# Kernel optimization log

Hardware: AMD Instinct MI355X
Metric: run time of the kernel (lower is better)

## Reference

```python
import jax, jax.numpy as jnp
import numpy as np
from jax import lax

# ---- config (mirrors init_kwargs) ----
B, CIN, T, WIDTH = 32, 8, 256, 128
COUT = 64
K = (5, 5)
PAD = (2, 2)            # ceil((k-1)*dilation/2) per dim
OUT_W = 128             # output_shape
EPS = 1e-8
BETA0 = 0.9             # beta 'constant' init, one_per_layer
B0 = 1.0                # b 'constant' init
SIGMA0 = 10.0
MAX_SPK = 3.0           # Max_spikes_per_run


@jax.custom_vjp
def spike_fn(mthr, sigma):
    # Surrogate Heaviside: hard threshold fwd, sigmoid-derivative surrogate bwd.
    return (mthr > 0).astype(mthr.dtype)

def _spike_fwd(mthr, sigma):
    return spike_fn(mthr, sigma), (mthr, sigma)

def _spike_bwd(res, g):
    mthr, sigma = res
    sg = jax.nn.sigmoid(sigma * mthr)
    return (g * sigma * sg * (1.0 - sg), jnp.zeros_like(sigma))

spike_fn.defvjp(_spike_fwd, _spike_bwd)


def setup_inputs() -> dict:
    key = jax.random.key(0)
    kx, kw = jax.random.split(key)
    x = jax.random.normal(kx, (B, CIN, T, WIDTH), dtype=jnp.float32)
    w_std = 1.0 * np.sqrt(1.0 / (CIN * K[0] * K[1]))
    w = jax.random.normal(kw, (COUT, CIN, K[0], K[1]), dtype=jnp.float32) * w_std
    b = jnp.full((COUT,), B0, dtype=jnp.float32)          # clamped >= 0
    beta = jnp.array([BETA0], dtype=jnp.float32)           # one_per_layer, clamped to [0,1]
    sigma = jnp.array([SIGMA0], dtype=jnp.float32)         # surrogate_sigma_mode 'one'
    return {"x": x, "w": w, "b": b, "beta": beta, "sigma": sigma}


def _forward(x, w, b, beta, sigma):
    # conv over (time, width) with 'same'-style padding, then truncate width
    conv_x = lax.conv_general_dilated(
        x, w, window_strides=(1, 1),
        padding=((PAD[0], PAD[0]), (PAD[1], PAD[1])),
        rhs_dilation=(1, 1),
        dimension_numbers=("NCHW", "OIHW", "NCHW"))
    conv_x = conv_x[:, :, :, :OUT_W]                      # [B, COUT, T, OUT_W]

    d = jnp.einsum("oikl,eikl->oe", w, w)                 # lateral matrix [COUT, COUT]
    norm = jnp.sum(w * w, axis=(1, 2, 3))                 # [COUT]
    inv_norm = 1.0 / (norm + EPS)
    beta_s = beta[0]

    conv_seq = jnp.transpose(conv_x, (2, 0, 1, 3))        # [T, B, COUT, OUT_W]

    def step(carry, inp_t):
        mem, spk, prev = carry
        rst = jnp.einsum("bcw,cd->bdw", spk, d)           # lateral reset
        # Leaky neuron, soft reset
        mem = (mem - rst) * beta_s + inp_t * (1.0 - beta_s)
        mthr = mem * inv_norm[None, :, None] - b[None, :, None]
        s = (MAX_SPK - prev) * spike_fn(mthr, sigma)      # spike_limit=True
        prev = prev + s
        return (mem, s, prev), s

    zeros = jnp.zeros((B, COUT, OUT_W), dtype=x.dtype)
    (_, _, _), spk_rec = lax.scan(step, (zeros, zeros, zeros), conv_seq)
    # spk_rec: [T, B, COUT, OUT_W]

    loss = 0.5 * jnp.mean(spk_rec ** 2)                   # 'squared'
    spk_spread = jnp.max(jnp.sum(spk_rec, axis=(1, 2, 3))) / (B * COUT * OUT_W)  # 'max'

    output = jnp.transpose(spk_rec, (1, 2, 0, 3))         # [B, COUT, T, OUT_W]
    return output, loss, spk_spread


def reference(x, w, b, beta, sigma):
    return _forward(x, w, b, beta, sigma)
```

## Files before the change

kernel.cpp:

```cpp
#include <hip/hip_runtime.h>
#include <cstdint>
#include <math.h>


#define NB 32
#define NC 8
#define NT 256
#define NW 128
#define NO 64
#define WT 16
#define TC 8
#define NROWS 12
#define NCHUNK (NT / TC)
#define XCOLS 20
#define XTILE (NC * NROWS * XCOLS)

__global__ __launch_bounds__(1024)
void prep_kernel(const float* __restrict__ w, float* __restrict__ d3,
                 float* __restrict__ invn, unsigned int* __restrict__ gfires)
{
    __shared__ float wsh[NO * 200];
    const int tid = threadIdx.x;
    for (int i = tid; i < NO * 200; i += 1024) wsh[i] = w[i];
    if (tid < NT) gfires[tid] = 0u;
    __syncthreads();
#pragma unroll
    for (int p = 0; p < 4; ++p) {
        int idx = p * 1024 + tid;
        int o = idx >> 6, e = idx & 63;
        float acc = 0.0f;
        for (int i = 0; i < 200; i += 4) {
            float4 av = *(const float4*)&wsh[o * 200 + i];
            float4 bv = *(const float4*)&wsh[e * 200 + i];
            acc += av.x * bv.x + av.y * bv.y + av.z * bv.z + av.w * bv.w;
        }
        d3[idx] = 3.0f * acc;
        if (o == e) invn[o] = 1.0f / (acc + 1e-8f);
    }
}

__global__ __launch_bounds__(512, 1)
void spk_kernel(const float* __restrict__ x, const float* __restrict__ wglob,
                const float* __restrict__ bias, const float* __restrict__ beta_p,
                const float* __restrict__ d3g, const float* __restrict__ invng,
                float* __restrict__ out, unsigned int* __restrict__ gfires)
{
    __shared__ float wsm[NC * 25 * NO];
    __shared__ float d3s[NO * NO];
    __shared__ float xsh[2][NC][NROWS][XCOLS];
    __shared__ unsigned short tf[2][NO][8];
    __shared__ unsigned int sf[NT];

    const int tid  = threadIdx.x;
    const int lane = tid & 63;
    const int wv   = tid >> 6;
    const int bb   = blockIdx.x >> 3;
    const int w0   = (blockIdx.x & 7) * WT;

    for (int i = tid; i < NC * 25 * NO; i += 512) {
        int co = i & 63; int r = i >> 6;
        int kw = r % 5; int r2 = r / 5; int kt = r2 % 5; int c = r2 / 5;
        wsm[i] = wglob[((co * NC + c) * 5 + kt) * 5 + kw];
    }
    for (int i = tid; i < NO * NO; i += 512) d3s[i] = d3g[i];
    for (int i = tid; i < NT; i += 512) sf[i] = 0u;

    const size_t xbbase = (size_t)bb * NC * NT * NW;

    const float* pf_ptr[4];
    int  pf_idx[4];
    int  pf_row[4];
    bool pf_okw[4];
#pragma unroll
    for (int k = 0; k < 4; ++k) {
        int i = tid + k * 512;
        if (i < XTILE) {
            int c = i / (NROWS * XCOLS); int rem = i - c * (NROWS * XCOLS);
            int row = rem / XCOLS; int col = rem - row * XCOLS;
            int wg = w0 + col - 2;
            pf_idx[k] = i; pf_row[k] = row;
            pf_okw[k] = (wg >= 0 && wg < NW);
            pf_ptr[k] = x + xbbase + ((size_t)c * NT + 6 + row) * NW + (wg < 0 ? 0 : wg);
        } else { pf_idx[k] = -1; pf_row[k] = 0; pf_okw[k] = false; pf_ptr[k] = x; }
    }

    const int sq = tid & 3;
    const int srow = tid >> 2;
    int    sp_tfidx[4];
    int    sp_tt[4];
    float* sp_out[4];
#pragma unroll
    for (int p = 0; p < 4; ++p) {
        int rowi = p * 128 + srow;
        int co = rowi >> 3, tt = rowi & 7;
        sp_tfidx[p] = co * 8 + sq * 2;
        sp_tt[p] = tt;
        sp_out[p] = out + (((size_t)(bb * NO + co) * NT + tt) * NW + w0 + sq * 4);
    }

#pragma unroll
    for (int k = 0; k < 4; ++k) {
        int i = tid + k * 512;
        if (i < XTILE) {
            int c = i / (NROWS * XCOLS); int rem = i - c * (NROWS * XCOLS);
            int row = rem / XCOLS; int col = rem - row * XCOLS;
            int tg = row - 2, wg = w0 + col - 2;
            float v = 0.0f;
            if (tg >= 0 && tg < NT && wg >= 0 && wg < NW)
                v = x[xbbase + ((size_t)c * NT + tg) * NW + wg];
            (&xsh[0][0][0][0])[i] = v;
        }
    }

    const float invn = invng[lane];
    const float bco  = bias[lane];
    const float beta = beta_p[0];
    const float omb  = 1.0f - beta;

    float mem0 = 0.f, mem1 = 0.f;
    unsigned int fired = 0u;
    unsigned long long pm0 = 0ull, pm1 = 0ull;

    __syncthreads();

#pragma unroll 1
    for (int ch = 0; ch < NCHUNK; ++ch) {
        const int buf = ch & 1;
        const int tbase = ch * TC;

        float sr[4];
        if (ch + 1 < NCHUNK) {
#pragma unroll
            for (int k = 0; k < 4; ++k) {
                float v = 0.0f;
                int tg = (ch << 3) + 6 + pf_row[k];
                if (pf_okw[k] && tg < NT)
                    v = pf_ptr[k][(size_t)ch * (TC * NW)];
                sr[k] = v;
            }
        }

        if (ch > 0) {
            const unsigned short* tfp = &tf[buf ^ 1][0][0];
            const size_t oadv = (size_t)(ch - 1) * (TC * NW);
#pragma unroll
            for (int p = 0; p < 4; ++p) {
                unsigned int codes = *(const unsigned int*)(tfp + sp_tfidx[p]);
                unsigned int tt = (unsigned)sp_tt[p];
                float4 v;
                v.x = (((codes      ) & 0xffu) == tt) ? 3.0f : 0.0f;
                v.y = (((codes >>  8) & 0xffu) == tt) ? 3.0f : 0.0f;
                v.z = (((codes >> 16) & 0xffu) == tt) ? 3.0f : 0.0f;
                v.w = (((codes >> 24) & 0xffu) == tt) ? 3.0f : 0.0f;
                *(float4*)(sp_out[p] + oadv) = v;
            }
        }

        float acc[TC][2];
#pragma unroll
        for (int t = 0; t < TC; ++t) { acc[t][0] = 0.f; acc[t][1] = 0.f; }

#pragma unroll 2
        for (int c = 0; c < NC; ++c) {
            float2 xr[NROWS][3];
#pragma unroll
            for (int r = 0; r < NROWS; ++r) {
                const float* base = &xsh[buf][c][r][2 * wv];
                xr[r][0] = *(const float2*)(base);
                xr[r][1] = *(const float2*)(base + 2);
                xr[r][2] = *(const float2*)(base + 4);
            }
#pragma unroll
            for (int kt = 0; kt < 5; ++kt) {
                const float* wp = &wsm[((c * 5 + kt) * 5) * 64 + lane];
                float wk0 = wp[0], wk1 = wp[64], wk2 = wp[128], wk3 = wp[192], wk4 = wp[256];
#pragma unroll
                for (int t = 0; t < TC; ++t) {
                    float2 a = xr[t + kt][0], b2 = xr[t + kt][1], c2 = xr[t + kt][2];
                    float u0 = acc[t][0], u1 = acc[t][1];
                    u0 = fmaf(wk0, a.x,  u0);
                    u0 = fmaf(wk1, a.y,  u0);
                    u0 = fmaf(wk2, b2.x, u0);
                    u0 = fmaf(wk3, b2.y, u0);
                    u0 = fmaf(wk4, c2.x, u0);
                    u1 = fmaf(wk0, a.y,  u1);
                    u1 = fmaf(wk1, b2.x, u1);
                    u1 = fmaf(wk2, b2.y, u1);
                    u1 = fmaf(wk3, c2.x, u1);
                    u1 = fmaf(wk4, c2.y, u1);
                    acc[t][0] = u0; acc[t][1] = u1;
                }
            }
        }

        unsigned int tfc0 = 0xffu, tfc1 = 0xffu;
#pragma unroll
        for (int tt = 0; tt < TC; ++tt) {
            float r0 = 0.f, r1 = 0.f;
            if (pm0 | pm1) {
                unsigned long long m = pm0;
                while (m) { int c = __builtin_ctzll(m); m &= m - 1; r0 += d3s[c * 64 + lane]; }
                m = pm1;
                while (m) { int c = __builtin_ctzll(m); m &= m - 1; r1 += d3s[c * 64 + lane]; }
            }
            mem0 = (mem0 - r0) * beta + acc[tt][0] * omb;
            mem1 = (mem1 - r1) * beta + acc[tt][1] * omb;
            bool f0 = !(fired & 1u) && (mem0 * invn - bco > 0.0f);
            bool f1 = !(fired & 2u) && (mem1 * invn - bco > 0.0f);
            pm0 = __ballot(f0);
            pm1 = __ballot(f1);
            if (f0) { fired |= 1u; tfc0 = (unsigned)tt; }
            if (f1) { fired |= 2u; tfc1 = (unsigned)tt; }
            unsigned int cnt = (unsigned)(__popcll(pm0) + __popcll(pm1));
            if (lane == 0 && cnt) atomicAdd(&sf[tbase + tt], cnt);
        }
        tf[buf][lane][wv] = (unsigned short)(tfc0 | (tfc1 << 8));

        if (ch + 1 < NCHUNK) {
            float* dst = &xsh[buf ^ 1][0][0][0];
#pragma unroll
            for (int k = 0; k < 4; ++k) {
                if (pf_idx[k] >= 0) dst[pf_idx[k]] = sr[k];
            }
        }
        __syncthreads();
    }

    {
        const unsigned short* tfp = &tf[(NCHUNK - 1) & 1][0][0];
        const size_t oadv = (size_t)(NCHUNK - 1) * (TC * NW);
#pragma unroll
        for (int p = 0; p < 4; ++p) {
            unsigned int codes = *(const unsigned int*)(tfp + sp_tfidx[p]);
            unsigned int tt = (unsigned)sp_tt[p];
            float4 v;
            v.x = (((codes      ) & 0xffu) == tt) ? 3.0f : 0.0f;
            v.y = (((codes >>  8) & 0xffu) == tt) ? 3.0f : 0.0f;
            v.z = (((codes >> 16) & 0xffu) == tt) ? 3.0f : 0.0f;
            v.w = (((codes >> 24) & 0xffu) == tt) ? 3.0f : 0.0f;
            *(float4*)(sp_out[p] + oadv) = v;
        }
    }

    if (tid < NT) atomicAdd(&gfires[tid], sf[tid]);
}

__global__ __launch_bounds__(256)
void fin_kernel(const unsigned int* __restrict__ gfires, float* __restrict__ out)
{
    const int tid = threadIdx.x;
    unsigned int v = gfires[tid];
    unsigned int s = v, m = v;
    for (int off = 32; off > 0; off >>= 1) {
        s += __shfl_down(s, off);
        unsigned int o = __shfl_down(m, off);
        m = m > o ? m : o;
    }
    __shared__ unsigned int ls[4], lm[4];
    if ((tid & 63) == 0) { ls[tid >> 6] = s; lm[tid >> 6] = m; }
    __syncthreads();
    if (tid == 0) {
        unsigned int ts = 0, tm = 0;
        for (int i = 0; i < 4; ++i) { ts += ls[i]; tm = tm > lm[i] ? tm : lm[i]; }
        out[67108864] = 4.5f * (float)ts / 67108864.0f;
        out[67108865] = 3.0f * (float)tm / 262144.0f;
    }
}

extern "C" void kernel_launch(void* const* d_in, const int* in_sizes, int n_in,
                              void* d_out, int out_size, void* d_ws, size_t ws_size,
                              hipStream_t stream)
{
    const float* x    = (const float*)d_in[0];
    const float* w    = (const float*)d_in[1];
    const float* b    = (const float*)d_in[2];
    const float* beta = (const float*)d_in[3];

    float* out  = (float*)d_out;
    float* wsf  = (float*)d_ws;
    float* d3   = wsf;
    float* invn = wsf + 4096;
    unsigned int* gf = (unsigned int*)(wsf + 4160);

    prep_kernel<<<1, 1024, 0, stream>>>(w, d3, invn, gf);
    spk_kernel<<<256, 512, 0, stream>>>(x, w, b, beta, d3, invn, out, gf);
    fin_kernel<<<1, 256, 0, stream>>>(gf, out);
}
```

Measured before the change: 752.8 us.

## Double-buffer conv operands in registers, split prep across blocks, allow two blocks/CU

The per-channel convolution loop now preloads the next channel's x rows and 25 weights into registers while computing the current one, a software-pipelining step meant to hide LDS latency. The prep kernel is spread over 16 blocks instead of one so computing the lateral matrix is parallel. The spk kernel's launch bounds now request two blocks per CU, which caps registers per thread. That cap could cause spills given the larger register footprint of the double buffers.

```diff
diff --git a/kernel.cpp b/kernel.cpp
--- a/kernel.cpp
+++ b/kernel.cpp
@@ -15,20 +15,64 @@
 #define XCOLS 20
 #define XTILE (NC * NROWS * XCOLS)
 
+__device__ __forceinline__ void loadx(float2 (&dst)[NROWS][3], const float* base)
+{
+#pragma unroll
+    for (int r = 0; r < NROWS; ++r) {
+        dst[r][0] = *(const float2*)(base + r * XCOLS);
+        dst[r][1] = *(const float2*)(base + r * XCOLS + 2);
+        dst[r][2] = *(const float2*)(base + r * XCOLS + 4);
+    }
+}
+
+__device__ __forceinline__ void loadw(float (&dst)[25], const float* wbase)
+{
+#pragma unroll
+    for (int i = 0; i < 25; ++i) dst[i] = wbase[i * 64];
+}
+
+__device__ __forceinline__ void fmablk(float (&acc)[TC][2],
+                                       const float2 (&xr)[NROWS][3],
+                                       const float (&wv_)[25])
+{
+#pragma unroll
+    for (int kt = 0; kt < 5; ++kt) {
+        float wk0 = wv_[kt * 5 + 0], wk1 = wv_[kt * 5 + 1], wk2 = wv_[kt * 5 + 2];
+        float wk3 = wv_[kt * 5 + 3], wk4 = wv_[kt * 5 + 4];
+#pragma unroll
+        for (int t = 0; t < TC; ++t) {
+            float2 a = xr[t + kt][0], b2 = xr[t + kt][1], c2 = xr[t + kt][2];
+            float u0 = acc[t][0], u1 = acc[t][1];
+            u0 = fmaf(wk0, a.x,  u0);
+            u0 = fmaf(wk1, a.y,  u0);
+            u0 = fmaf(wk2, b2.x, u0);
+            u0 = fmaf(wk3, b2.y, u0);
+            u0 = fmaf(wk4, c2.x, u0);
+            u1 = fmaf(wk0, a.y,  u1);
+            u1 = fmaf(wk1, b2.x, u1);
+            u1 = fmaf(wk2, b2.y, u1);
+            u1 = fmaf(wk3, c2.x, u1);
+            u1 = fmaf(wk4, c2.y, u1);
+            acc[t][0] = u0; acc[t][1] = u1;
+        }
+    }
+}
+
 __global__ __launch_bounds__(1024)
 void prep_kernel(const float* __restrict__ w, float* __restrict__ d3,
                  float* __restrict__ invn, unsigned int* __restrict__ gfires)
 {
     __shared__ float wsh[NO * 200];
     const int tid = threadIdx.x;
+    const int bid = blockIdx.x;
     for (int i = tid; i < NO * 200; i += 1024) wsh[i] = w[i];
-    if (tid < NT) gfires[tid] = 0u;
+    if (bid == 0 && tid < NT) gfires[tid] = 0u;
     __syncthreads();
-#pragma unroll
-    for (int p = 0; p < 4; ++p) {
-        int idx = p * 1024 + tid;
+    if (tid < 256) {
+        int idx = bid * 256 + tid;
         int o = idx >> 6, e = idx & 63;
         float acc = 0.0f;
+#pragma unroll
         for (int i = 0; i < 200; i += 4) {
             float4 av = *(const float4*)&wsh[o * 200 + i];
             float4 bv = *(const float4*)&wsh[e * 200 + i];
@@ -39,7 +83,7 @@
     }
 }
 
-__global__ __launch_bounds__(512, 1)
+__global__ __launch_bounds__(512, 2)
 void spk_kernel(const float* __restrict__ x, const float* __restrict__ wglob,
                 const float* __restrict__ bias, const float* __restrict__ beta_p,
                 const float* __restrict__ d3g, const float* __restrict__ invng,
@@ -160,36 +204,22 @@
 #pragma unroll
         for (int t = 0; t < TC; ++t) { acc[t][0] = 0.f; acc[t][1] = 0.f; }
 
-#pragma unroll 2
-        for (int c = 0; c < NC; ++c) {
-            float2 xr[NROWS][3];
-#pragma unroll
-            for (int r = 0; r < NROWS; ++r) {
-                const float* base = &xsh[buf][c][r][2 * wv];
-                xr[r][0] = *(const float2*)(base);
-                xr[r][1] = *(const float2*)(base + 2);
-                xr[r][2] = *(const float2*)(base + 4);
-            }
-#pragma unroll
-            for (int kt = 0; kt < 5; ++kt) {
-                const float* wp = &wsm[((c * 5 + kt) * 5) * 64 + lane];
-                float wk0 = wp[0], wk1 = wp[64], wk2 = wp[128], wk3 = wp[192], wk4 = wp[256];
-#pragma unroll
-                for (int t = 0; t < TC; ++t) {
-                    float2 a = xr[t + kt][0], b2 = xr[t + kt][1], c2 = xr[t + kt][2];
-                    float u0 = acc[t][0], u1 = acc[t][1];
-                    u0 = fmaf(wk0, a.x,  u0);
-                    u0 = fmaf(wk1, a.y,  u0);
-                    u0 = fmaf(wk2, b2.x, u0);
-                    u0 = fmaf(wk3, b2.y, u0);
-                    u0 = fmaf(wk4, c2.x, u0);
-                    u1 = fmaf(wk0, a.y,  u1);
-                    u1 = fmaf(wk1, b2.x, u1);
-                    u1 = fmaf(wk2, b2.y, u1);
-                    u1 = fmaf(wk3, c2.x, u1);
-                    u1 = fmaf(wk4, c2.y, u1);
-                    acc[t][0] = u0; acc[t][1] = u1;
+        const float* xb = &xsh[buf][0][0][0] + 2 * wv;
+        {
+            float2 xA[NROWS][3]; float wA[25];
+            loadx(xA, xb);
+            loadw(wA, &wsm[lane]);
+#pragma unroll 1
+            for (int cc = 0; cc < 4; ++cc) {
+                float2 xB[NROWS][3]; float wB[25];
+                loadx(xB, xb + (2 * cc + 1) * (NROWS * XCOLS));
+                loadw(wB, &wsm[(2 * cc + 1) * 25 * 64 + lane]);
+                fmablk(acc, xA, wA);
+                if (cc < 3) {
+                    loadx(xA, xb + (2 * cc + 2) * (NROWS * XCOLS));
+                    loadw(wA, &wsm[(2 * cc + 2) * 25 * 64 + lane]);
                 }
+                fmablk(acc, xB, wB);
             }
         }
 
@@ -282,7 +312,7 @@
     float* invn = wsf + 4096;
     unsigned int* gf = (unsigned int*)(wsf + 4160);
 
-    prep_kernel<<<1, 1024, 0, stream>>>(w, d3, invn, gf);
+    prep_kernel<<<16, 1024, 0, stream>>>(w, d3, invn, gf);
     spk_kernel<<<256, 512, 0, stream>>>(x, w, b, beta, d3, invn, out, gf);
     fin_kernel<<<1, 256, 0, stream>>>(gf, out);
 }
```

New measurement: 2.959 ms. +293.1%, slower.

## Use 1024 threads with one width column per wave; split prep across blocks

Applied to the files above, without the earlier changes.

The spike kernel now launches 1024 threads per block, so each of the 16 waves owns a single width column instead of two. This halves the per-thread convolution and scan work and doubles wave-level parallelism on the serial time recurrence. The lateral-reset loop, spike-code storage (now byte-wide) and output store indexing are resized to match. The prep kernel is split over 16 blocks of 256 active threads to compute the lateral matrix in parallel. The trade-off is that the shared x tile is reloaded per column by more waves, the c loop is no longer unrolled, and register pressure under the 1024-thread launch bound may limit scheduling.

```diff
diff --git a/kernel.cpp b/kernel.cpp
--- a/kernel.cpp
+++ b/kernel.cpp
@@ -21,14 +21,15 @@
 {
     __shared__ float wsh[NO * 200];
     const int tid = threadIdx.x;
+    const int bid = blockIdx.x;
     for (int i = tid; i < NO * 200; i += 1024) wsh[i] = w[i];
-    if (tid < NT) gfires[tid] = 0u;
+    if (bid == 0 && tid < NT) gfires[tid] = 0u;
     __syncthreads();
-#pragma unroll
-    for (int p = 0; p < 4; ++p) {
-        int idx = p * 1024 + tid;
+    if (tid < 256) {
+        int idx = bid * 256 + tid;
         int o = idx >> 6, e = idx & 63;
         float acc = 0.0f;
+#pragma unroll
         for (int i = 0; i < 200; i += 4) {
             float4 av = *(const float4*)&wsh[o * 200 + i];
             float4 bv = *(const float4*)&wsh[e * 200 + i];
@@ -39,7 +40,7 @@
     }
 }
 
-__global__ __launch_bounds__(512, 1)
+__global__ __launch_bounds__(1024, 1)
 void spk_kernel(const float* __restrict__ x, const float* __restrict__ wglob,
                 const float* __restrict__ bias, const float* __restrict__ beta_p,
                 const float* __restrict__ d3g, const float* __restrict__ invng,
@@ -48,7 +49,7 @@
     __shared__ float wsm[NC * 25 * NO];
     __shared__ float d3s[NO * NO];
     __shared__ float xsh[2][NC][NROWS][XCOLS];
-    __shared__ unsigned short tf[2][NO][8];
+    __shared__ unsigned char tf[2][NO][16];
     __shared__ unsigned int sf[NT];
 
     const int tid  = threadIdx.x;
@@ -57,23 +58,23 @@
     const int bb   = blockIdx.x >> 3;
     const int w0   = (blockIdx.x & 7) * WT;
 
-    for (int i = tid; i < NC * 25 * NO; i += 512) {
+    for (int i = tid; i < NC * 25 * NO; i += 1024) {
         int co = i & 63; int r = i >> 6;
         int kw = r % 5; int r2 = r / 5; int kt = r2 % 5; int c = r2 / 5;
         wsm[i] = wglob[((co * NC + c) * 5 + kt) * 5 + kw];
     }
-    for (int i = tid; i < NO * NO; i += 512) d3s[i] = d3g[i];
-    for (int i = tid; i < NT; i += 512) sf[i] = 0u;
+    for (int i = tid; i < NO * NO; i += 1024) d3s[i] = d3g[i];
+    if (tid < NT) sf[tid] = 0u;
 
     const size_t xbbase = (size_t)bb * NC * NT * NW;
 
-    const float* pf_ptr[4];
-    int  pf_idx[4];
-    int  pf_row[4];
-    bool pf_okw[4];
-#pragma unroll
-    for (int k = 0; k < 4; ++k) {
-        int i = tid + k * 512;
+    const float* pf_ptr[2];
+    int  pf_idx[2];
+    int  pf_row[2];
+    bool pf_okw[2];
+#pragma unroll
+    for (int k = 0; k < 2; ++k) {
+        int i = tid + k * 1024;
         if (i < XTILE) {
             int c = i / (NROWS * XCOLS); int rem = i - c * (NROWS * XCOLS);
             int row = rem / XCOLS; int col = rem - row * XCOLS;
@@ -86,21 +87,21 @@
 
     const int sq = tid & 3;
     const int srow = tid >> 2;
-    int    sp_tfidx[4];
-    int    sp_tt[4];
-    float* sp_out[4];
-#pragma unroll
-    for (int p = 0; p < 4; ++p) {
-        int rowi = p * 128 + srow;
+    int    sp_tfidx[2];
+    int    sp_tt[2];
+    float* sp_out[2];
+#pragma unroll
+    for (int p = 0; p < 2; ++p) {
+        int rowi = p * 256 + srow;
         int co = rowi >> 3, tt = rowi & 7;
-        sp_tfidx[p] = co * 8 + sq * 2;
+        sp_tfidx[p] = co * 16 + sq * 4;
         sp_tt[p] = tt;
         sp_out[p] = out + (((size_t)(bb * NO + co) * NT + tt) * NW + w0 + sq * 4);
     }
 
 #pragma unroll
-    for (int k = 0; k < 4; ++k) {
-        int i = tid + k * 512;
+    for (int k = 0; k < 2; ++k) {
+        int i = tid + k * 1024;
         if (i < XTILE) {
             int c = i / (NROWS * XCOLS); int rem = i - c * (NROWS * XCOLS);
             int row = rem / XCOLS; int col = rem - row * XCOLS;
@@ -117,9 +118,9 @@
     const float beta = beta_p[0];
     const float omb  = 1.0f - beta;
 
-    float mem0 = 0.f, mem1 = 0.f;
-    unsigned int fired = 0u;
-    unsigned long long pm0 = 0ull, pm1 = 0ull;
+    float mem0 = 0.f;
+    bool fired = false;
+    unsigned long long pm0 = 0ull;
 
     __syncthreads();
 
@@ -128,10 +129,10 @@
         const int buf = ch & 1;
         const int tbase = ch * TC;
 
-        float sr[4];
+        float sr[2];
         if (ch + 1 < NCHUNK) {
 #pragma unroll
-            for (int k = 0; k < 4; ++k) {
+            for (int k = 0; k < 2; ++k) {
                 float v = 0.0f;
                 int tg = (ch << 3) + 6 + pf_row[k];
                 if (pf_okw[k] && tg < NT)
@@ -141,10 +142,10 @@
         }
 
         if (ch > 0) {
-            const unsigned short* tfp = &tf[buf ^ 1][0][0];
+            const unsigned char* tfp = &tf[buf ^ 1][0][0];
             const size_t oadv = (size_t)(ch - 1) * (TC * NW);
 #pragma unroll
-            for (int p = 0; p < 4; ++p) {
+            for (int p = 0; p < 2; ++p) {
                 unsigned int codes = *(const unsigned int*)(tfp + sp_tfidx[p]);
                 unsigned int tt = (unsigned)sp_tt[p];
                 float4 v;
@@ -156,19 +157,18 @@
             }
         }
 
-        float acc[TC][2];
-#pragma unroll
-        for (int t = 0; t < TC; ++t) { acc[t][0] = 0.f; acc[t][1] = 0.f; }
-
-#pragma unroll 2
+        float acc[TC];
+#pragma unroll
+        for (int t = 0; t < TC; ++t) acc[t] = 0.f;
+
+#pragma unroll 1
         for (int c = 0; c < NC; ++c) {
-            float2 xr[NROWS][3];
+            float xr[NROWS][5];
 #pragma unroll
             for (int r = 0; r < NROWS; ++r) {
-                const float* base = &xsh[buf][c][r][2 * wv];
-                xr[r][0] = *(const float2*)(base);
-                xr[r][1] = *(const float2*)(base + 2);
-                xr[r][2] = *(const float2*)(base + 4);
+#pragma unroll
+                for (int j = 0; j < 5; ++j)
+                    xr[r][j] = xsh[buf][c][r][wv + j];
             }
 #pragma unroll
             for (int kt = 0; kt < 5; ++kt) {
@@ -176,50 +176,38 @@
                 float wk0 = wp[0], wk1 = wp[64], wk2 = wp[128], wk3 = wp[192], wk4 = wp[256];
 #pragma unroll
                 for (int t = 0; t < TC; ++t) {
-                    float2 a = xr[t + kt][0], b2 = xr[t + kt][1], c2 = xr[t + kt][2];
-                    float u0 = acc[t][0], u1 = acc[t][1];
-                    u0 = fmaf(wk0, a.x,  u0);
-                    u0 = fmaf(wk1, a.y,  u0);
-                    u0 = fmaf(wk2, b2.x, u0);
-                    u0 = fmaf(wk3, b2.y, u0);
-                    u0 = fmaf(wk4, c2.x, u0);
-                    u1 = fmaf(wk0, a.y,  u1);
-                    u1 = fmaf(wk1, b2.x, u1);
-                    u1 = fmaf(wk2, b2.y, u1);
-                    u1 = fmaf(wk3, c2.x, u1);
-                    u1 = fmaf(wk4, c2.y, u1);
-                    acc[t][0] = u0; acc[t][1] = u1;
+                    float u = acc[t];
+                    u = fmaf(wk0, xr[t + kt][0], u);
+                    u = fmaf(wk1, xr[t + kt][1], u);
+                    u = fmaf(wk2, xr[t + kt][2], u);
+                    u = fmaf(wk3, xr[t + kt][3], u);
+                    u = fmaf(wk4, xr[t + kt][4], u);
+                    acc[t] = u;
                 }
             }
         }
 
-        unsigned int tfc0 = 0xffu, tfc1 = 0xffu;
+        unsigned int tfc0 = 0xffu;
 #pragma unroll
         for (int tt = 0; tt < TC; ++tt) {
-            float r0 = 0.f, r1 = 0.f;
-            if (pm0 | pm1) {
+            float r0 = 0.f;
+            if (pm0) {
                 unsigned long long m = pm0;
                 while (m) { int c = __builtin_ctzll(m); m &= m - 1; r0 += d3s[c * 64 + lane]; }
-                m = pm1;
-                while (m) { int c = __builtin_ctzll(m); m &= m - 1; r1 += d3s[c * 64 + lane]; }
-            }
-            mem0 = (mem0 - r0) * beta + acc[tt][0] * omb;
-            mem1 = (mem1 - r1) * beta + acc[tt][1] * omb;
-            bool f0 = !(fired & 1u) && (mem0 * invn - bco > 0.0f);
-            bool f1 = !(fired & 2u) && (mem1 * invn - bco > 0.0f);
+            }
+            mem0 = (mem0 - r0) * beta + acc[tt] * omb;
+            bool f0 = !fired && (mem0 * invn - bco > 0.0f);
             pm0 = __ballot(f0);
-            pm1 = __ballot(f1);
-            if (f0) { fired |= 1u; tfc0 = (unsigned)tt; }
-            if (f1) { fired |= 2u; tfc1 = (unsigned)tt; }
-            unsigned int cnt = (unsigned)(__popcll(pm0) + __popcll(pm1));
+            if (f0) { fired = true; tfc0 = (unsigned)tt; }
+            unsigned int cnt = (unsigned)__popcll(pm0);
             if (lane == 0 && cnt) atomicAdd(&sf[tbase + tt], cnt);
         }
-        tf[buf][lane][wv] = (unsigned short)(tfc0 | (tfc1 << 8));
+        tf[buf][lane][wv] = (unsigned char)tfc0;
 
         if (ch + 1 < NCHUNK) {
             float* dst = &xsh[buf ^ 1][0][0][0];
 #pragma unroll
-            for (int k = 0; k < 4; ++k) {
+            for (int k = 0; k < 2; ++k) {
                 if (pf_idx[k] >= 0) dst[pf_idx[k]] = sr[k];
             }
         }
@@ -227,10 +215,10 @@
     }
 
     {
-        const unsigned short* tfp = &tf[(NCHUNK - 1) & 1][0][0];
+        const unsigned char* tfp = &tf[(NCHUNK - 1) & 1][0][0];
         const size_t oadv = (size_t)(NCHUNK - 1) * (TC * NW);
 #pragma unroll
-        for (int p = 0; p < 4; ++p) {
+        for (int p = 0; p < 2; ++p) {
             unsigned int codes = *(const unsigned int*)(tfp + sp_tfidx[p]);
             unsigned int tt = (unsigned)sp_tt[p];
             float4 v;
@@ -282,7 +270,7 @@
     float* invn = wsf + 4096;
     unsigned int* gf = (unsigned int*)(wsf + 4160);
 
-    prep_kernel<<<1, 1024, 0, stream>>>(w, d3, invn, gf);
-    spk_kernel<<<256, 512, 0, stream>>>(x, w, b, beta, d3, invn, out, gf);
+    prep_kernel<<<16, 1024, 0, stream>>>(w, d3, invn, gf);
+    spk_kernel<<<256, 1024, 0, stream>>>(x, w, b, beta, d3, invn, out, gf);
     fin_kernel<<<1, 256, 0, stream>>>(gf, out);
 }
```

Measured after the change: 854.2 us. 13.5% more time.
